# Optimization experiments

Measured on AMD Instinct MI355X. Metric: run time of the kernel, lower is better.

Reference implementation:

```python
import jax, jax.numpy as jnp
import numpy as np

B, N, K, C, CE, H = 2, 2048, 48, 128, 128, 128
IN = 2 * C + CE  # 384
AGG_SCALE = 30.0
LN_EPS = 1e-5


def setup_inputs() -> dict:
    key = jax.random.key(0)
    ks = jax.random.split(key, 12)
    inp = {
        "node_h": jax.random.normal(ks[0], (B, N, C), jnp.float32),
        "edge_h": jax.random.normal(ks[1], (B, N, K, CE), jnp.float32),
        "edge_index": jax.random.randint(ks[2], (B, N, K), 0, N, jnp.int64),
        # message MLP: Linear(IN,H) GELU Linear(H,H) GELU Linear(H,C)
        "W1": jax.random.normal(ks[3], (IN, H), jnp.float32) / np.sqrt(IN),
        "b1": jnp.zeros((H,), jnp.float32),
        "W2": jax.random.normal(ks[4], (H, H), jnp.float32) / np.sqrt(H),
        "b2": jnp.zeros((H,), jnp.float32),
        "W3": jax.random.normal(ks[5], (H, C), jnp.float32) / np.sqrt(H),
        "b3": jnp.zeros((C,), jnp.float32),
        "Wu": jax.random.normal(ks[6], (C, C), jnp.float32) / np.sqrt(C),
        "bu": jnp.zeros((C,), jnp.float32),
        "ln_g": jnp.ones((C,), jnp.float32),
        "ln_b": jnp.zeros((C,), jnp.float32),
    }
    return inp


def _layer_norm(x, g, b):
    mu = jnp.mean(x, axis=-1, keepdims=True)
    var = jnp.var(x, axis=-1, keepdims=True)
    return (x - mu) * jax.lax.rsqrt(var + LN_EPS) * g + b


def _gelu(x):
    return jax.nn.gelu(x, approximate=False)  # torch nn.GELU default (erf)


def reference(node_h, edge_h, edge_index, W1, b1, W2, b2, W3, b3, Wu, bu, ln_g, ln_b):
    b, n, k = edge_index.shape
    c = node_h.shape[-1]
    # gather neighbor node features: (B,N,K,C)
    node_j = jnp.take_along_axis(
        node_h, edge_index.reshape(b, n * k)[..., None], axis=1
    ).reshape(b, n, k, c)
    node_i = jnp.broadcast_to(node_h[:, :, None, :], (b, n, k, c))
    edge_packed = jnp.concatenate([node_i, node_j, edge_h], axis=-1)  # (B,N,K,IN)
    # message MLP
    h = _gelu(edge_packed @ W1 + b1)
    h = _gelu(h @ W2 + b2)
    messages = (h @ W3 + b3).sum(axis=-2) / AGG_SCALE  # (B,N,C)
    # dropout is identity in eval mode
    updated_nodes = _layer_norm(node_h + messages, ln_g, ln_b)
    node_updates = updated_nodes @ Wu + bu
    out = _layer_norm(node_h + node_updates, ln_g, ln_b)
    return out
```

## Files before the change

### kernel.cpp

```cpp
#include <hip/hip_runtime.h>
#include <hip/hip_bf16.h>
#include <math.h>

#define Bn   2
#define Nn   2048
#define Kn   48
#define Cn   128
#define G2   16

typedef short bf16x8 __attribute__((ext_vector_type(8)));
typedef float f32x4  __attribute__((ext_vector_type(4)));

#if __has_builtin(__builtin_amdgcn_cvt_pk_bf16_f32)
#define HAS_PK 1
#endif

__device__ __forceinline__ short f2bf(float f) {
  union { float f; unsigned u; } v; v.f = f;
  unsigned r = v.u + 0x7fffu + ((v.u >> 16) & 1u);
  return (short)(r >> 16);
}

__device__ __forceinline__ unsigned pk2(float a, float b) {
#ifdef HAS_PK
  auto p = __builtin_amdgcn_cvt_pk_bf16_f32(a, b);
  return __builtin_bit_cast(unsigned, p);
#else
  return (unsigned)(unsigned short)f2bf(a) | ((unsigned)(unsigned short)f2bf(b) << 16);
#endif
}

__device__ __forceinline__ float gelu_f(float x) {
  float z = x * (-2.3021991f - 0.10294200f * x * x);
  float e = __builtin_amdgcn_exp2f(z);
  return x * __builtin_amdgcn_rcpf(1.0f + e);
}

__global__ void pack_weights(const float* __restrict__ W1,
                             const float* __restrict__ W2,
                             const float* __restrict__ W3,
                             const float* __restrict__ Wu,
                             short* __restrict__ ws) {
  int tid = blockIdx.x * blockDim.x + threadIdx.x;
  if (tid >= 192 * 64) return;
  int lane = tid & 63;
  int tile = tid >> 6;
  const float* W; short* dst;
  if (tile < 32)       { W = W1;         dst = ws; }
  else if (tile < 96)  { W = W1 + 16384; dst = ws + 16384; tile -= 32; }
  else if (tile < 128) { W = W2;         dst = ws + 49152; tile -= 96; }
  else if (tile < 160) { W = W3;         dst = ws + 65536; tile -= 128; }
  else                 { W = Wu;         dst = ws + 81920; tile -= 160; }
  int kt = tile >> 3, nt = tile & 7;
  int n  = nt * 16 + (lane & 15);
  int k0 = kt * 32 + (lane >> 4) * 8;
  union { short s[8]; bf16x8 v; } u8;
#pragma unroll
  for (int j = 0; j < 8; j++) u8.s[j] = f2bf(W[(k0 + j) * 128 + n]);
  *reinterpret_cast<bf16x8*>(dst + (tile << 9) + lane * 8) = u8.v;
}

__global__ __launch_bounds__(256, 6)
void node_update_kernel(const float* __restrict__ node_h,
                        const float* __restrict__ edge_h,
                        const int*   __restrict__ edge_index,
                        const short* __restrict__ wpack,
                        const float* __restrict__ b1,
                        const float* __restrict__ b2,
                        float* __restrict__ hs_out) {
  __shared__ __align__(16) char smem[25024];
  short* Xs    = (short*)smem;
  short* H1s   = (short*)(smem + 12288);
  short* nhb   = (short*)(smem + 24576);
  int*   idx_s = (int*)  (smem + 24832);

  const int tid  = threadIdx.x;
  const int blk  = blockIdx.x;
  const int bb   = blk >> 11;
  const int lane = tid & 63;
  const int wave = tid >> 6;
  const int lr   = lane & 15;
  const int lq   = lane >> 4;

  const short* W1i = wpack;
  const short* W1e = wpack + 16384;
  const short* W2p = wpack + 49152;

  if (tid < 128) {
    nhb[tid] = f2bf(node_h[(size_t)blk * Cn + tid]);
  } else if (tid < 176) {
    idx_s[tid - 128] = edge_index[blk * Kn + (tid - 128)];
  }
  __syncthreads();

  {
    const int w  = tid & 31;
    const int rr = tid >> 5;
#pragma unroll
    for (int k = 0; k < 6; k++) {
      int r = rr + k * 8;
      const float* src = (w < 16)
          ? node_h + (size_t)(bb * Nn + idx_s[r]) * Cn + w * 8
          : edge_h + ((size_t)blk * Kn + r) * Cn + (w - 16) * 8;
      float4 v0 = *reinterpret_cast<const float4*>(src);
      float4 v1 = *reinterpret_cast<const float4*>(src + 4);
      uint4 p;
      p.x = pk2(v0.x, v0.y); p.y = pk2(v0.z, v0.w);
      p.z = pk2(v1.x, v1.y); p.w = pk2(v1.z, v1.w);
      *reinterpret_cast<uint4*>(&Xs[r * 256 + ((w ^ (r & 7)) << 3)]) = p;
    }
  }

  f32x4 accY[2] = {};
#pragma unroll
  for (int kt = 0; kt < 4; kt++) {
    bf16x8 av = {};
    if (lr == 0) av = *reinterpret_cast<const bf16x8*>(&nhb[kt * 32 + lq * 8]);
    bf16x8 bv0 = *reinterpret_cast<const bf16x8*>(W1i + ((kt * 8 + wave * 2 + 0) << 9) + lane * 8);
    bf16x8 bv1 = *reinterpret_cast<const bf16x8*>(W1i + ((kt * 8 + wave * 2 + 1) << 9) + lane * 8);
    accY[0] = __builtin_amdgcn_mfma_f32_16x16x32_bf16(av, bv0, accY[0], 0, 0, 0);
    accY[1] = __builtin_amdgcn_mfma_f32_16x16x32_bf16(av, bv1, accY[1], 0, 0, 0);
  }
  __syncthreads();

  f32x4 acc[3][2] = {};
#pragma unroll
  for (int kt = 0; kt < 8; kt++) {
    bf16x8 bf0 = *reinterpret_cast<const bf16x8*>(W1e + ((kt * 8 + wave * 2 + 0) << 9) + lane * 8);
    bf16x8 bf1 = *reinterpret_cast<const bf16x8*>(W1e + ((kt * 8 + wave * 2 + 1) << 9) + lane * 8);
    int sw = (((kt * 4 + lq) ^ (lr & 7)) << 3);
    bf16x8 a0 = *reinterpret_cast<const bf16x8*>(&Xs[(0  + lr) * 256 + sw]);
    bf16x8 a1 = *reinterpret_cast<const bf16x8*>(&Xs[(16 + lr) * 256 + sw]);
    bf16x8 a2 = *reinterpret_cast<const bf16x8*>(&Xs[(32 + lr) * 256 + sw]);
    acc[0][0] = __builtin_amdgcn_mfma_f32_16x16x32_bf16(a0, bf0, acc[0][0], 0, 0, 0);
    acc[0][1] = __builtin_amdgcn_mfma_f32_16x16x32_bf16(a0, bf1, acc[0][1], 0, 0, 0);
    acc[1][0] = __builtin_amdgcn_mfma_f32_16x16x32_bf16(a1, bf0, acc[1][0], 0, 0, 0);
    acc[1][1] = __builtin_amdgcn_mfma_f32_16x16x32_bf16(a1, bf1, acc[1][1], 0, 0, 0);
    acc[2][0] = __builtin_amdgcn_mfma_f32_16x16x32_bf16(a2, bf0, acc[2][0], 0, 0, 0);
    acc[2][1] = __builtin_amdgcn_mfma_f32_16x16x32_bf16(a2, bf1, acc[2][1], 0, 0, 0);
  }
  __syncthreads();

#pragma unroll
  for (int j = 0; j < 2; j++) {
    int col = (wave * 2 + j) * 16 + lr;
    float yi = __shfl(accY[j][0], lr) + b1[col];
    int g = col >> 3, cl = col & 7;
#pragma unroll
    for (int mt = 0; mt < 3; mt++) {
      int r0 = mt * 16 + lq * 4;
      float g0 = gelu_f(acc[mt][j][0] + yi);
      float g1 = gelu_f(acc[mt][j][1] + yi);
      float g2 = gelu_f(acc[mt][j][2] + yi);
      float g3 = gelu_f(acc[mt][j][3] + yi);
      unsigned p01 = pk2(g0, g1), p23 = pk2(g2, g3);
      H1s[(r0 + 0) * 128 + ((g ^ ((r0 + 0) & 7)) << 3) + cl] = (short)(p01 & 0xffff);
      H1s[(r0 + 1) * 128 + ((g ^ ((r0 + 1) & 7)) << 3) + cl] = (short)(p01 >> 16);
      H1s[(r0 + 2) * 128 + ((g ^ ((r0 + 2) & 7)) << 3) + cl] = (short)(p23 & 0xffff);
      H1s[(r0 + 3) * 128 + ((g ^ ((r0 + 3) & 7)) << 3) + cl] = (short)(p23 >> 16);
    }
  }
  __syncthreads();

  f32x4 acc2[3][2] = {};
#pragma unroll
  for (int kt = 0; kt < 4; kt++) {
    bf16x8 bf0 = *reinterpret_cast<const bf16x8*>(W2p + ((kt * 8 + wave * 2 + 0) << 9) + lane * 8);
    bf16x8 bf1 = *reinterpret_cast<const bf16x8*>(W2p + ((kt * 8 + wave * 2 + 1) << 9) + lane * 8);
    int sw = (((kt * 4 + lq) ^ (lr & 7)) << 3);
    bf16x8 a0 = *reinterpret_cast<const bf16x8*>(&H1s[(0  + lr) * 128 + sw]);
    bf16x8 a1 = *reinterpret_cast<const bf16x8*>(&H1s[(16 + lr) * 128 + sw]);
    bf16x8 a2 = *reinterpret_cast<const bf16x8*>(&H1s[(32 + lr) * 128 + sw]);
    acc2[0][0] = __builtin_amdgcn_mfma_f32_16x16x32_bf16(a0, bf0, acc2[0][0], 0, 0, 0);
    acc2[0][1] = __builtin_amdgcn_mfma_f32_16x16x32_bf16(a0, bf1, acc2[0][1], 0, 0, 0);
    acc2[1][0] = __builtin_amdgcn_mfma_f32_16x16x32_bf16(a1, bf0, acc2[1][0], 0, 0, 0);
    acc2[1][1] = __builtin_amdgcn_mfma_f32_16x16x32_bf16(a1, bf1, acc2[1][1], 0, 0, 0);
    acc2[2][0] = __builtin_amdgcn_mfma_f32_16x16x32_bf16(a2, bf0, acc2[2][0], 0, 0, 0);
    acc2[2][1] = __builtin_amdgcn_mfma_f32_16x16x32_bf16(a2, bf1, acc2[2][1], 0, 0, 0);
  }
#pragma unroll
  for (int j = 0; j < 2; j++) {
    int col = (wave * 2 + j) * 16 + lr;
    float bias = b2[col];
    float s = 0.f;
#pragma unroll
    for (int mt = 0; mt < 3; mt++)
#pragma unroll
      for (int r = 0; r < 4; r++) s += gelu_f(acc2[mt][j][r] + bias);
    s += __shfl_xor(s, 16);
    s += __shfl_xor(s, 32);
    if (lq == 0) hs_out[(size_t)blk * Cn + col] = s;
  }
}

__global__ __launch_bounds__(256, 4)
void tail_kernel(const float* __restrict__ node_h,
                 const short* __restrict__ wpack,
                 const float* __restrict__ b3,
                 const float* __restrict__ bu,
                 const float* __restrict__ ln_g,
                 const float* __restrict__ ln_b,
                 float* __restrict__ out) {
  __shared__ __align__(16) char sm2[24832];
  short* hsB = (short*)sm2;
  float* nhr = (float*)(sm2 + 4096);
  float* xs  = (float*)(sm2 + 12288);
  short* usB = (short*)(sm2 + 20736);

  const int tid  = threadIdx.x;
  const int lane = tid & 63;
  const int wave = tid >> 6;
  const int lr   = lane & 15;
  const int lq   = lane >> 4;
  const int n0   = blockIdx.x * G2;

  const short* W3p = wpack + 65536;
  const short* Wup = wpack + 81920;

  {
    int row = tid >> 4, seg = tid & 15;
    const float* p = node_h + (size_t)(n0 + row) * Cn + seg * 8;
    float4 a0 = *reinterpret_cast<const float4*>(p);
    float4 a1 = *reinterpret_cast<const float4*>(p + 4);
    *reinterpret_cast<float4*>(&nhr[row * 128 + seg * 8])     = a0;
    *reinterpret_cast<float4*>(&nhr[row * 128 + seg * 8 + 4]) = a1;
    const float* q = out + (size_t)(n0 + row) * Cn + seg * 8;
    float4 c0 = *reinterpret_cast<const float4*>(q);
    float4 c1 = *reinterpret_cast<const float4*>(q + 4);
    uint4 pk;
    pk.x = pk2(c0.x, c0.y); pk.y = pk2(c0.z, c0.w);
    pk.z = pk2(c1.x, c1.y); pk.w = pk2(c1.z, c1.w);
    *reinterpret_cast<uint4*>(&hsB[row * 128 + ((seg ^ (row & 7)) << 3)]) = pk;
  }
  __syncthreads();

  f32x4 am[2] = {};
#pragma unroll
  for (int kt = 0; kt < 4; kt++) {
    bf16x8 av = *reinterpret_cast<const bf16x8*>(&hsB[lr * 128 + (((kt * 4 + lq) ^ (lr & 7)) << 3)]);
    bf16x8 bv0 = *reinterpret_cast<const bf16x8*>(W3p + ((kt * 8 + wave * 2 + 0) << 9) + lane * 8);
    bf16x8 bv1 = *reinterpret_cast<const bf16x8*>(W3p + ((kt * 8 + wave * 2 + 1) << 9) + lane * 8);
    am[0] = __builtin_amdgcn_mfma_f32_16x16x32_bf16(av, bv0, am[0], 0, 0, 0);
    am[1] = __builtin_amdgcn_mfma_f32_16x16x32_bf16(av, bv1, am[1], 0, 0, 0);
  }
#pragma unroll
  for (int j = 0; j < 2; j++) {
    int col = (wave * 2 + j) * 16 + lr;
    float bb = 48.0f * b3[col];
#pragma unroll
    for (int r = 0; r < 4; r++) {
      int row = lq * 4 + r;
      xs[row * 132 + col] = nhr[row * 128 + col] + (am[j][r] + bb) * (1.0f / 30.0f);
    }
  }
  __syncthreads();

  const float lg1 = ln_g[lane],      lb1v = ln_b[lane];
  const float lg2 = ln_g[lane + 64], lb2v = ln_b[lane + 64];
#pragma unroll
  for (int s = 0; s < 4; s++) {
    int row = wave * 4 + s;
    float v1 = xs[row * 132 + lane];
    float v2 = xs[row * 132 + lane + 64];
    float s1 = v1 + v2, s2 = v1 * v1 + v2 * v2;
#pragma unroll
    for (int off = 32; off >= 1; off >>= 1) {
      s1 += __shfl_xor(s1, off);
      s2 += __shfl_xor(s2, off);
    }
    float mu = s1 * (1.f / 128.f);
    float var = s2 * (1.f / 128.f) - mu * mu;
    float rstd = rsqrtf(var + 1e-5f);
    unsigned u12 = pk2((v1 - mu) * rstd * lg1 + lb1v,
                       (v2 - mu) * rstd * lg2 + lb2v);
    int sw = (row & 7);
    usB[row * 128 + (((lane >> 3) ^ sw) << 3) + (lane & 7)]       = (short)(u12 & 0xffff);
    usB[row * 128 + ((((lane >> 3) + 8) ^ sw) << 3) + (lane & 7)] = (short)(u12 >> 16);
  }
  __syncthreads();

  f32x4 au[2] = {};
#pragma unroll
  for (int kt = 0; kt < 4; kt++) {
    bf16x8 av = *reinterpret_cast<const bf16x8*>(&usB[lr * 128 + (((kt * 4 + lq) ^ (lr & 7)) << 3)]);
    bf16x8 bv0 = *reinterpret_cast<const bf16x8*>(Wup + ((kt * 8 + wave * 2 + 0) << 9) + lane * 8);
    bf16x8 bv1 = *reinterpret_cast<const bf16x8*>(Wup + ((kt * 8 + wave * 2 + 1) << 9) + lane * 8);
    au[0] = __builtin_amdgcn_mfma_f32_16x16x32_bf16(av, bv0, au[0], 0, 0, 0);
    au[1] = __builtin_amdgcn_mfma_f32_16x16x32_bf16(av, bv1, au[1], 0, 0, 0);
  }
  __syncthreads();
#pragma unroll
  for (int j = 0; j < 2; j++) {
    int col = (wave * 2 + j) * 16 + lr;
    float bb = bu[col];
#pragma unroll
    for (int r = 0; r < 4; r++) {
      int row = lq * 4 + r;
      xs[row * 132 + col] = nhr[row * 128 + col] + au[j][r] + bb;
    }
  }
  __syncthreads();

#pragma unroll
  for (int s = 0; s < 4; s++) {
    int row = wave * 4 + s;
    float v1 = xs[row * 132 + lane];
    float v2 = xs[row * 132 + lane + 64];
    float s1 = v1 + v2, s2 = v1 * v1 + v2 * v2;
#pragma unroll
    for (int off = 32; off >= 1; off >>= 1) {
      s1 += __shfl_xor(s1, off);
      s2 += __shfl_xor(s2, off);
    }
    float mu = s1 * (1.f / 128.f);
    float var = s2 * (1.f / 128.f) - mu * mu;
    float rstd = rsqrtf(var + 1e-5f);
    out[(size_t)(n0 + row) * Cn + lane]      = (v1 - mu) * rstd * lg1 + lb1v;
    out[(size_t)(n0 + row) * Cn + lane + 64] = (v2 - mu) * rstd * lg2 + lb2v;
  }
}

extern "C" void kernel_launch(void* const* d_in, const int* in_sizes, int n_in,
                              void* d_out, int out_size, void* d_ws, size_t ws_size,
                              hipStream_t stream) {
  const float* node_h     = (const float*)d_in[0];
  const float* edge_h     = (const float*)d_in[1];
  const int*   edge_index = (const int*)  d_in[2];
  const float* W1 = (const float*)d_in[3];
  const float* b1 = (const float*)d_in[4];
  const float* W2 = (const float*)d_in[5];
  const float* b2 = (const float*)d_in[6];
  const float* W3 = (const float*)d_in[7];
  const float* b3 = (const float*)d_in[8];
  const float* Wu = (const float*)d_in[9];
  const float* bu = (const float*)d_in[10];
  const float* ln_g = (const float*)d_in[11];
  const float* ln_b = (const float*)d_in[12];
  float* out   = (float*)d_out;
  short* wpack = (short*)d_ws;

  pack_weights<<<48, 256, 0, stream>>>(W1, W2, W3, Wu, wpack);
  node_update_kernel<<<Bn * Nn, 256, 0, stream>>>(
      node_h, edge_h, edge_index, wpack, b1, b2, out);
  tail_kernel<<<(Bn * Nn) / G2, 256, 0, stream>>>(
      node_h, wpack, b3, bu, ln_g, ln_b, out);
}
```

Before: 204.6 us.

## Prefetch weights into registers and double-buffer LDS operands in node kernel

```diff
diff --git a/kernel.cpp b/kernel.cpp
--- a/kernel.cpp
+++ b/kernel.cpp
@@ -60,7 +60,7 @@
   *reinterpret_cast<bf16x8*>(dst + (tile << 9) + lane * 8) = u8.v;
 }
 
-__global__ __launch_bounds__(256, 6)
+__global__ __launch_bounds__(256, 4)
 void node_update_kernel(const float* __restrict__ node_h,
                         const float* __restrict__ edge_h,
                         const int*   __restrict__ edge_index,
@@ -68,11 +68,9 @@
                         const float* __restrict__ b1,
                         const float* __restrict__ b2,
                         float* __restrict__ hs_out) {
-  __shared__ __align__(16) char smem[25024];
-  short* Xs    = (short*)smem;
-  short* H1s   = (short*)(smem + 12288);
-  short* nhb   = (short*)(smem + 24576);
-  int*   idx_s = (int*)  (smem + 24832);
+  __shared__ __align__(16) char smem[24576];
+  short* Xs  = (short*)smem;
+  short* H1s = (short*)(smem + 12288);
 
   const int tid  = threadIdx.x;
   const int blk  = blockIdx.x;
@@ -86,58 +84,98 @@
   const short* W1e = wpack + 16384;
   const short* W2p = wpack + 49152;
 
-  if (tid < 128) {
-    nhb[tid] = f2bf(node_h[(size_t)blk * Cn + tid]);
-  } else if (tid < 176) {
-    idx_s[tid - 128] = edge_index[blk * Kn + (tid - 128)];
-  }
-  __syncthreads();
-
+  const int w  = tid & 31;
+  const int rr = tid >> 5;
+  int idxv[6];
+  if (w < 16) {
+#pragma unroll
+    for (int k = 0; k < 6; k++)
+      idxv[k] = edge_index[blk * Kn + rr + k * 8];
+  }
+
+  bf16x8 avk[4] = {{0}, {0}, {0}, {0}};
+  if (lr == 0) {
+    const float* p = node_h + (size_t)blk * Cn;
+#pragma unroll
+    for (int kt = 0; kt < 4; kt++) {
+      float4 a0 = *reinterpret_cast<const float4*>(p + kt * 32 + lq * 8);
+      float4 a1 = *reinterpret_cast<const float4*>(p + kt * 32 + lq * 8 + 4);
+      union { unsigned u[4]; bf16x8 v; } q;
+      q.u[0] = pk2(a0.x, a0.y); q.u[1] = pk2(a0.z, a0.w);
+      q.u[2] = pk2(a1.x, a1.y); q.u[3] = pk2(a1.z, a1.w);
+      avk[kt] = q.v;
+    }
+  }
+
+  f32x4 accY[2] = {};
   {
-    const int w  = tid & 31;
-    const int rr = tid >> 5;
-#pragma unroll
-    for (int k = 0; k < 6; k++) {
-      int r = rr + k * 8;
-      const float* src = (w < 16)
-          ? node_h + (size_t)(bb * Nn + idx_s[r]) * Cn + w * 8
-          : edge_h + ((size_t)blk * Kn + r) * Cn + (w - 16) * 8;
-      float4 v0 = *reinterpret_cast<const float4*>(src);
-      float4 v1 = *reinterpret_cast<const float4*>(src + 4);
-      uint4 p;
-      p.x = pk2(v0.x, v0.y); p.y = pk2(v0.z, v0.w);
-      p.z = pk2(v1.x, v1.y); p.w = pk2(v1.z, v1.w);
-      *reinterpret_cast<uint4*>(&Xs[r * 256 + ((w ^ (r & 7)) << 3)]) = p;
-    }
-  }
-
-  f32x4 accY[2] = {};
-#pragma unroll
-  for (int kt = 0; kt < 4; kt++) {
-    bf16x8 av = {};
-    if (lr == 0) av = *reinterpret_cast<const bf16x8*>(&nhb[kt * 32 + lq * 8]);
-    bf16x8 bv0 = *reinterpret_cast<const bf16x8*>(W1i + ((kt * 8 + wave * 2 + 0) << 9) + lane * 8);
-    bf16x8 bv1 = *reinterpret_cast<const bf16x8*>(W1i + ((kt * 8 + wave * 2 + 1) << 9) + lane * 8);
-    accY[0] = __builtin_amdgcn_mfma_f32_16x16x32_bf16(av, bv0, accY[0], 0, 0, 0);
-    accY[1] = __builtin_amdgcn_mfma_f32_16x16x32_bf16(av, bv1, accY[1], 0, 0, 0);
+    bf16x8 bi[4];
+#pragma unroll
+    for (int kt = 0; kt < 4; kt++) {
+      int t = kt * 8 + wave * 2;
+      bi[kt] = *reinterpret_cast<const bf16x8*>(W1i + (t << 9) + lane * 8);
+    }
+#pragma unroll
+    for (int kt = 0; kt < 4; kt++) {
+      int t = kt * 8 + wave * 2;
+      bf16x8 bj = *reinterpret_cast<const bf16x8*>(W1i + ((t + 1) << 9) + lane * 8);
+      accY[0] = __builtin_amdgcn_mfma_f32_16x16x32_bf16(avk[kt], bi[kt], accY[0], 0, 0, 0);
+      accY[1] = __builtin_amdgcn_mfma_f32_16x16x32_bf16(avk[kt], bj, accY[1], 0, 0, 0);
+    }
+  }
+
+#pragma unroll
+  for (int k = 0; k < 6; k++) {
+    int r = rr + k * 8;
+    const float* src = (w < 16)
+        ? node_h + (size_t)(bb * Nn + idxv[k]) * Cn + w * 8
+        : edge_h + ((size_t)blk * Kn + r) * Cn + (w - 16) * 8;
+    float4 v0 = *reinterpret_cast<const float4*>(src);
+    float4 v1 = *reinterpret_cast<const float4*>(src + 4);
+    uint4 p;
+    p.x = pk2(v0.x, v0.y); p.y = pk2(v0.z, v0.w);
+    p.z = pk2(v1.x, v1.y); p.w = pk2(v1.z, v1.w);
+    *reinterpret_cast<uint4*>(&Xs[r * 256 + ((w ^ (r & 7)) << 3)]) = p;
+  }
+
+  bf16x8 Bf[16];
+#pragma unroll
+  for (int t = 0; t < 16; t++) {
+    int tile = (t >> 1) * 8 + wave * 2 + (t & 1);
+    Bf[t] = *reinterpret_cast<const bf16x8*>(W1e + (tile << 9) + lane * 8);
   }
   __syncthreads();
 
   f32x4 acc[3][2] = {};
-#pragma unroll
-  for (int kt = 0; kt < 8; kt++) {
-    bf16x8 bf0 = *reinterpret_cast<const bf16x8*>(W1e + ((kt * 8 + wave * 2 + 0) << 9) + lane * 8);
-    bf16x8 bf1 = *reinterpret_cast<const bf16x8*>(W1e + ((kt * 8 + wave * 2 + 1) << 9) + lane * 8);
-    int sw = (((kt * 4 + lq) ^ (lr & 7)) << 3);
-    bf16x8 a0 = *reinterpret_cast<const bf16x8*>(&Xs[(0  + lr) * 256 + sw]);
-    bf16x8 a1 = *reinterpret_cast<const bf16x8*>(&Xs[(16 + lr) * 256 + sw]);
-    bf16x8 a2 = *reinterpret_cast<const bf16x8*>(&Xs[(32 + lr) * 256 + sw]);
-    acc[0][0] = __builtin_amdgcn_mfma_f32_16x16x32_bf16(a0, bf0, acc[0][0], 0, 0, 0);
-    acc[0][1] = __builtin_amdgcn_mfma_f32_16x16x32_bf16(a0, bf1, acc[0][1], 0, 0, 0);
-    acc[1][0] = __builtin_amdgcn_mfma_f32_16x16x32_bf16(a1, bf0, acc[1][0], 0, 0, 0);
-    acc[1][1] = __builtin_amdgcn_mfma_f32_16x16x32_bf16(a1, bf1, acc[1][1], 0, 0, 0);
-    acc[2][0] = __builtin_amdgcn_mfma_f32_16x16x32_bf16(a2, bf0, acc[2][0], 0, 0, 0);
-    acc[2][1] = __builtin_amdgcn_mfma_f32_16x16x32_bf16(a2, bf1, acc[2][1], 0, 0, 0);
+  {
+    int sw0 = ((lq ^ (lr & 7)) << 3);
+    bf16x8 a0 = *reinterpret_cast<const bf16x8*>(&Xs[(0  + lr) * 256 + sw0]);
+    bf16x8 a1 = *reinterpret_cast<const bf16x8*>(&Xs[(16 + lr) * 256 + sw0]);
+    bf16x8 a2 = *reinterpret_cast<const bf16x8*>(&Xs[(32 + lr) * 256 + sw0]);
+#pragma unroll
+    for (int kt = 0; kt < 8; kt++) {
+      bf16x8 n0, n1, n2;
+      if (kt < 7) {
+        int sw = ((((kt + 1) * 4 + lq) ^ (lr & 7)) << 3);
+        n0 = *reinterpret_cast<const bf16x8*>(&Xs[(0  + lr) * 256 + sw]);
+        n1 = *reinterpret_cast<const bf16x8*>(&Xs[(16 + lr) * 256 + sw]);
+        n2 = *reinterpret_cast<const bf16x8*>(&Xs[(32 + lr) * 256 + sw]);
+      }
+      acc[0][0] = __builtin_amdgcn_mfma_f32_16x16x32_bf16(a0, Bf[kt*2+0], acc[0][0], 0, 0, 0);
+      acc[0][1] = __builtin_amdgcn_mfma_f32_16x16x32_bf16(a0, Bf[kt*2+1], acc[0][1], 0, 0, 0);
+      acc[1][0] = __builtin_amdgcn_mfma_f32_16x16x32_bf16(a1, Bf[kt*2+0], acc[1][0], 0, 0, 0);
+      acc[1][1] = __builtin_amdgcn_mfma_f32_16x16x32_bf16(a1, Bf[kt*2+1], acc[1][1], 0, 0, 0);
+      acc[2][0] = __builtin_amdgcn_mfma_f32_16x16x32_bf16(a2, Bf[kt*2+0], acc[2][0], 0, 0, 0);
+      acc[2][1] = __builtin_amdgcn_mfma_f32_16x16x32_bf16(a2, Bf[kt*2+1], acc[2][1], 0, 0, 0);
+      a0 = n0; a1 = n1; a2 = n2;
+    }
+  }
+
+  bf16x8 B2[8];
+#pragma unroll
+  for (int t = 0; t < 8; t++) {
+    int tile = (t >> 1) * 8 + wave * 2 + (t & 1);
+    B2[t] = *reinterpret_cast<const bf16x8*>(W2p + (tile << 9) + lane * 8);
   }
   __syncthreads();
 
@@ -163,21 +201,30 @@
   __syncthreads();
 
   f32x4 acc2[3][2] = {};
-#pragma unroll
-  for (int kt = 0; kt < 4; kt++) {
-    bf16x8 bf0 = *reinterpret_cast<const bf16x8*>(W2p + ((kt * 8 + wave * 2 + 0) << 9) + lane * 8);
-    bf16x8 bf1 = *reinterpret_cast<const bf16x8*>(W2p + ((kt * 8 + wave * 2 + 1) << 9) + lane * 8);
-    int sw = (((kt * 4 + lq) ^ (lr & 7)) << 3);
-    bf16x8 a0 = *reinterpret_cast<const bf16x8*>(&H1s[(0  + lr) * 128 + sw]);
-    bf16x8 a1 = *reinterpret_cast<const bf16x8*>(&H1s[(16 + lr) * 128 + sw]);
-    bf16x8 a2 = *reinterpret_cast<const bf16x8*>(&H1s[(32 + lr) * 128 + sw]);
-    acc2[0][0] = __builtin_amdgcn_mfma_f32_16x16x32_bf16(a0, bf0, acc2[0][0], 0, 0, 0);
-    acc2[0][1] = __builtin_amdgcn_mfma_f32_16x16x32_bf16(a0, bf1, acc2[0][1], 0, 0, 0);
-    acc2[1][0] = __builtin_amdgcn_mfma_f32_16x16x32_bf16(a1, bf0, acc2[1][0], 0, 0, 0);
-    acc2[1][1] = __builtin_amdgcn_mfma_f32_16x16x32_bf16(a1, bf1, acc2[1][1], 0, 0, 0);
-    acc2[2][0] = __builtin_amdgcn_mfma_f32_16x16x32_bf16(a2, bf0, acc2[2][0], 0, 0, 0);
-    acc2[2][1] = __builtin_amdgcn_mfma_f32_16x16x32_bf16(a2, bf1, acc2[2][1], 0, 0, 0);
-  }
+  {
+    int sw0 = ((lq ^ (lr & 7)) << 3);
+    bf16x8 a0 = *reinterpret_cast<const bf16x8*>(&H1s[(0  + lr) * 128 + sw0]);
+    bf16x8 a1 = *reinterpret_cast<const bf16x8*>(&H1s[(16 + lr) * 128 + sw0]);
+    bf16x8 a2 = *reinterpret_cast<const bf16x8*>(&H1s[(32 + lr) * 128 + sw0]);
+#pragma unroll
+    for (int kt = 0; kt < 4; kt++) {
+      bf16x8 n0, n1, n2;
+      if (kt < 3) {
+        int sw = ((((kt + 1) * 4 + lq) ^ (lr & 7)) << 3);
+        n0 = *reinterpret_cast<const bf16x8*>(&H1s[(0  + lr) * 128 + sw]);
+        n1 = *reinterpret_cast<const bf16x8*>(&H1s[(16 + lr) * 128 + sw]);
+        n2 = *reinterpret_cast<const bf16x8*>(&H1s[(32 + lr) * 128 + sw]);
+      }
+      acc2[0][0] = __builtin_amdgcn_mfma_f32_16x16x32_bf16(a0, B2[kt*2+0], acc2[0][0], 0, 0, 0);
+      acc2[0][1] = __builtin_amdgcn_mfma_f32_16x16x32_bf16(a0, B2[kt*2+1], acc2[0][1], 0, 0, 0);
+      acc2[1][0] = __builtin_amdgcn_mfma_f32_16x16x32_bf16(a1, B2[kt*2+0], acc2[1][0], 0, 0, 0);
+      acc2[1][1] = __builtin_amdgcn_mfma_f32_16x16x32_bf16(a1, B2[kt*2+1], acc2[1][1], 0, 0, 0);
+      acc2[2][0] = __builtin_amdgcn_mfma_f32_16x16x32_bf16(a2, B2[kt*2+0], acc2[2][0], 0, 0, 0);
+      acc2[2][1] = __builtin_amdgcn_mfma_f32_16x16x32_bf16(a2, B2[kt*2+1], acc2[2][1], 0, 0, 0);
+      a0 = n0; a1 = n1; a2 = n2;
+    }
+  }
+
 #pragma unroll
   for (int j = 0; j < 2; j++) {
     int col = (wave * 2 + j) * 16 + lr;
```

After: 211.6 us. 1.03x slower.

## Change LDS swizzle pattern, drop index staging barrier, load node row directly

Applied to the files above, without the earlier changes.

```diff
diff --git a/kernel.cpp b/kernel.cpp
--- a/kernel.cpp
+++ b/kernel.cpp
@@ -7,6 +7,8 @@
 #define Kn   48
 #define Cn   128
 #define G2   16
+
+#define SIG(r) ((((r) ^ ((r) >> 2))) & 7)
 
 typedef short bf16x8 __attribute__((ext_vector_type(8)));
 typedef float f32x4  __attribute__((ext_vector_type(4)));
@@ -68,11 +70,9 @@
                         const float* __restrict__ b1,
                         const float* __restrict__ b2,
                         float* __restrict__ hs_out) {
-  __shared__ __align__(16) char smem[25024];
-  short* Xs    = (short*)smem;
-  short* H1s   = (short*)(smem + 12288);
-  short* nhb   = (short*)(smem + 24576);
-  int*   idx_s = (int*)  (smem + 24832);
+  __shared__ __align__(16) char smem[24576];
+  short* Xs  = (short*)smem;
+  short* H1s = (short*)(smem + 12288);
 
   const int tid  = threadIdx.x;
   const int blk  = blockIdx.x;
@@ -86,52 +86,65 @@
   const short* W1e = wpack + 16384;
   const short* W2p = wpack + 49152;
 
-  if (tid < 128) {
-    nhb[tid] = f2bf(node_h[(size_t)blk * Cn + tid]);
-  } else if (tid < 176) {
-    idx_s[tid - 128] = edge_index[blk * Kn + (tid - 128)];
-  }
-  __syncthreads();
-
+  const int w  = tid & 31;
+  const int rr = tid >> 5;
+  int idxv[6];
+  if (w < 16) {
+#pragma unroll
+    for (int k = 0; k < 6; k++)
+      idxv[k] = edge_index[blk * Kn + rr + k * 8];
+  }
+
+  f32x4 accY[2] = {};
   {
-    const int w  = tid & 31;
-    const int rr = tid >> 5;
-#pragma unroll
-    for (int k = 0; k < 6; k++) {
-      int r = rr + k * 8;
-      const float* src = (w < 16)
-          ? node_h + (size_t)(bb * Nn + idx_s[r]) * Cn + w * 8
-          : edge_h + ((size_t)blk * Kn + r) * Cn + (w - 16) * 8;
-      float4 v0 = *reinterpret_cast<const float4*>(src);
-      float4 v1 = *reinterpret_cast<const float4*>(src + 4);
-      uint4 p;
-      p.x = pk2(v0.x, v0.y); p.y = pk2(v0.z, v0.w);
-      p.z = pk2(v1.x, v1.y); p.w = pk2(v1.z, v1.w);
-      *reinterpret_cast<uint4*>(&Xs[r * 256 + ((w ^ (r & 7)) << 3)]) = p;
-    }
-  }
-
-  f32x4 accY[2] = {};
-#pragma unroll
-  for (int kt = 0; kt < 4; kt++) {
-    bf16x8 av = {};
-    if (lr == 0) av = *reinterpret_cast<const bf16x8*>(&nhb[kt * 32 + lq * 8]);
-    bf16x8 bv0 = *reinterpret_cast<const bf16x8*>(W1i + ((kt * 8 + wave * 2 + 0) << 9) + lane * 8);
-    bf16x8 bv1 = *reinterpret_cast<const bf16x8*>(W1i + ((kt * 8 + wave * 2 + 1) << 9) + lane * 8);
-    accY[0] = __builtin_amdgcn_mfma_f32_16x16x32_bf16(av, bv0, accY[0], 0, 0, 0);
-    accY[1] = __builtin_amdgcn_mfma_f32_16x16x32_bf16(av, bv1, accY[1], 0, 0, 0);
-  }
-  __syncthreads();
-
+    bf16x8 avk[4] = {{0}, {0}, {0}, {0}};
+    if (lr == 0) {
+      const float* p = node_h + (size_t)blk * Cn;
+#pragma unroll
+      for (int kt = 0; kt < 4; kt++) {
+        float4 a0 = *reinterpret_cast<const float4*>(p + kt * 32 + lq * 8);
+        float4 a1 = *reinterpret_cast<const float4*>(p + kt * 32 + lq * 8 + 4);
+        union { unsigned u[4]; bf16x8 v; } q;
+        q.u[0] = pk2(a0.x, a0.y); q.u[1] = pk2(a0.z, a0.w);
+        q.u[2] = pk2(a1.x, a1.y); q.u[3] = pk2(a1.z, a1.w);
+        avk[kt] = q.v;
+      }
+    }
+#pragma unroll
+    for (int kt = 0; kt < 4; kt++) {
+      bf16x8 bv0 = *reinterpret_cast<const bf16x8*>(W1i + ((kt * 8 + wave * 2 + 0) << 9) + lane * 8);
+      bf16x8 bv1 = *reinterpret_cast<const bf16x8*>(W1i + ((kt * 8 + wave * 2 + 1) << 9) + lane * 8);
+      accY[0] = __builtin_amdgcn_mfma_f32_16x16x32_bf16(avk[kt], bv0, accY[0], 0, 0, 0);
+      accY[1] = __builtin_amdgcn_mfma_f32_16x16x32_bf16(avk[kt], bv1, accY[1], 0, 0, 0);
+    }
+  }
+
+#pragma unroll
+  for (int k = 0; k < 6; k++) {
+    int r = rr + k * 8;
+    const float* src = (w < 16)
+        ? node_h + (size_t)(bb * Nn + idxv[k]) * Cn + w * 8
+        : edge_h + ((size_t)blk * Kn + r) * Cn + (w - 16) * 8;
+    float4 v0 = *reinterpret_cast<const float4*>(src);
+    float4 v1 = *reinterpret_cast<const float4*>(src + 4);
+    uint4 p;
+    p.x = pk2(v0.x, v0.y); p.y = pk2(v0.z, v0.w);
+    p.z = pk2(v1.x, v1.y); p.w = pk2(v1.z, v1.w);
+    *reinterpret_cast<uint4*>(&Xs[r * 256 + ((w ^ SIG(r)) << 3)]) = p;
+  }
+  __syncthreads();
+
+  const int s0 = SIG(lr);
   f32x4 acc[3][2] = {};
 #pragma unroll
   for (int kt = 0; kt < 8; kt++) {
     bf16x8 bf0 = *reinterpret_cast<const bf16x8*>(W1e + ((kt * 8 + wave * 2 + 0) << 9) + lane * 8);
     bf16x8 bf1 = *reinterpret_cast<const bf16x8*>(W1e + ((kt * 8 + wave * 2 + 1) << 9) + lane * 8);
-    int sw = (((kt * 4 + lq) ^ (lr & 7)) << 3);
-    bf16x8 a0 = *reinterpret_cast<const bf16x8*>(&Xs[(0  + lr) * 256 + sw]);
-    bf16x8 a1 = *reinterpret_cast<const bf16x8*>(&Xs[(16 + lr) * 256 + sw]);
-    bf16x8 a2 = *reinterpret_cast<const bf16x8*>(&Xs[(32 + lr) * 256 + sw]);
+    int swA = (((kt * 4 + lq) ^ s0) << 3);
+    int swB = swA ^ (4 << 3);
+    bf16x8 a0 = *reinterpret_cast<const bf16x8*>(&Xs[(0  + lr) * 256 + swA]);
+    bf16x8 a1 = *reinterpret_cast<const bf16x8*>(&Xs[(16 + lr) * 256 + swB]);
+    bf16x8 a2 = *reinterpret_cast<const bf16x8*>(&Xs[(32 + lr) * 256 + swA]);
     acc[0][0] = __builtin_amdgcn_mfma_f32_16x16x32_bf16(a0, bf0, acc[0][0], 0, 0, 0);
     acc[0][1] = __builtin_amdgcn_mfma_f32_16x16x32_bf16(a0, bf1, acc[0][1], 0, 0, 0);
     acc[1][0] = __builtin_amdgcn_mfma_f32_16x16x32_bf16(a1, bf0, acc[1][0], 0, 0, 0);
@@ -141,23 +154,25 @@
   }
   __syncthreads();
 
+  const int s5 = (lq * 5) & 7;
 #pragma unroll
   for (int j = 0; j < 2; j++) {
     int col = (wave * 2 + j) * 16 + lr;
     float yi = __shfl(accY[j][0], lr) + b1[col];
-    int g = col >> 3, cl = col & 7;
+    int cl = col & 7;
 #pragma unroll
     for (int mt = 0; mt < 3; mt++) {
       int r0 = mt * 16 + lq * 4;
+      int gs = (col >> 3) ^ s5 ^ ((mt & 1) << 2);
       float g0 = gelu_f(acc[mt][j][0] + yi);
       float g1 = gelu_f(acc[mt][j][1] + yi);
       float g2 = gelu_f(acc[mt][j][2] + yi);
       float g3 = gelu_f(acc[mt][j][3] + yi);
       unsigned p01 = pk2(g0, g1), p23 = pk2(g2, g3);
-      H1s[(r0 + 0) * 128 + ((g ^ ((r0 + 0) & 7)) << 3) + cl] = (short)(p01 & 0xffff);
-      H1s[(r0 + 1) * 128 + ((g ^ ((r0 + 1) & 7)) << 3) + cl] = (short)(p01 >> 16);
-      H1s[(r0 + 2) * 128 + ((g ^ ((r0 + 2) & 7)) << 3) + cl] = (short)(p23 & 0xffff);
-      H1s[(r0 + 3) * 128 + ((g ^ ((r0 + 3) & 7)) << 3) + cl] = (short)(p23 >> 16);
+      H1s[(r0 + 0) * 128 + ((gs ^ 0) << 3) + cl] = (short)(p01 & 0xffff);
+      H1s[(r0 + 1) * 128 + ((gs ^ 1) << 3) + cl] = (short)(p01 >> 16);
+      H1s[(r0 + 2) * 128 + ((gs ^ 2) << 3) + cl] = (short)(p23 & 0xffff);
+      H1s[(r0 + 3) * 128 + ((gs ^ 3) << 3) + cl] = (short)(p23 >> 16);
     }
   }
   __syncthreads();
@@ -167,10 +182,11 @@
   for (int kt = 0; kt < 4; kt++) {
     bf16x8 bf0 = *reinterpret_cast<const bf16x8*>(W2p + ((kt * 8 + wave * 2 + 0) << 9) + lane * 8);
     bf16x8 bf1 = *reinterpret_cast<const bf16x8*>(W2p + ((kt * 8 + wave * 2 + 1) << 9) + lane * 8);
-    int sw = (((kt * 4 + lq) ^ (lr & 7)) << 3);
-    bf16x8 a0 = *reinterpret_cast<const bf16x8*>(&H1s[(0  + lr) * 128 + sw]);
-    bf16x8 a1 = *reinterpret_cast<const bf16x8*>(&H1s[(16 + lr) * 128 + sw]);
-    bf16x8 a2 = *reinterpret_cast<const bf16x8*>(&H1s[(32 + lr) * 128 + sw]);
+    int swA = (((kt * 4 + lq) ^ s0) << 3);
+    int swB = swA ^ (4 << 3);
+    bf16x8 a0 = *reinterpret_cast<const bf16x8*>(&H1s[(0  + lr) * 128 + swA]);
+    bf16x8 a1 = *reinterpret_cast<const bf16x8*>(&H1s[(16 + lr) * 128 + swB]);
+    bf16x8 a2 = *reinterpret_cast<const bf16x8*>(&H1s[(32 + lr) * 128 + swA]);
     acc2[0][0] = __builtin_amdgcn_mfma_f32_16x16x32_bf16(a0, bf0, acc2[0][0], 0, 0, 0);
     acc2[0][1] = __builtin_amdgcn_mfma_f32_16x16x32_bf16(a0, bf1, acc2[0][1], 0, 0, 0);
     acc2[1][0] = __builtin_amdgcn_mfma_f32_16x16x32_bf16(a1, bf0, acc2[1][0], 0, 0, 0);
```

Result: no change. 208.5 us (+1.9%).
